# Performance work log

Measured on AMD Instinct MI355X. Metric: run time of the kernel, lower is better.

Reference implementation:

```python
import jax, jax.numpy as jnp
import numpy as np

H = 512
IN_DIM = 300
NUM_CLASSES = 45
LN_EPS = 1e-5


def _ln(x, g, b):
    m = jnp.mean(x, axis=-1, keepdims=True)
    v = jnp.mean((x - m) ** 2, axis=-1, keepdims=True)
    return (x - m) / jnp.sqrt(v + LN_EPS) * g + b


def _rnn_dir(xemb, Wx, bx, Wh, bh, ln_g, ln_b):
    # xemb: [B, T, H]; Wx/Wh: [3, H, H]; bx/bh: [3, H]; ln_g/ln_b: [3, H]
    B = xemb.shape[0]
    h_init = (jnp.zeros((B, H), xemb.dtype),) * 3

    def step(carry, xt):
        h0, h1, h2 = carry
        h0 = jnp.tanh(_ln(xt @ Wx[0] + bx[0] + h0 @ Wh[0] + bh[0], ln_g[0], ln_b[0]))
        h1 = jnp.tanh(_ln(h0 @ Wx[1] + bx[1] + h1 @ Wh[1] + bh[1], ln_g[1], ln_b[1]))
        h2 = jnp.tanh(_ln(h1 @ Wx[2] + bx[2] + h2 @ Wh[2] + bh[2], ln_g[2], ln_b[2]))
        return (h0, h1, h2), h2

    _, ys = jax.lax.scan(step, h_init, jnp.swapaxes(xemb, 0, 1))  # ys: [T, B, H]
    return jnp.swapaxes(ys, 0, 1)  # [B, T, H]


def setup_inputs() -> dict:
    key = jax.random.key(0)
    ks = jax.random.split(key, 20)
    B, T = 128, 256
    s_in = 1.0 / np.sqrt(IN_DIM)
    s_h = 1.0 / np.sqrt(H)
    inp = {
        "x": jax.random.normal(ks[0], (B, T, IN_DIM), jnp.float32),
        "reverse_x": jax.random.normal(ks[1], (B, T, IN_DIM), jnp.float32),
        "pad_start_index": jax.random.randint(ks[2], (B,), 0, T),
        "max_length": T,
        "W_emb": jax.random.uniform(ks[3], (IN_DIM, H), jnp.float32, -s_in, s_in),
        "b_emb": jax.random.uniform(ks[4], (H,), jnp.float32, -s_in, s_in),
        "Wx_l2r": jax.random.uniform(ks[5], (3, H, H), jnp.float32, -s_h, s_h),
        "bx_l2r": jax.random.uniform(ks[6], (3, H), jnp.float32, -s_h, s_h),
        "Wh_l2r": jax.random.uniform(ks[7], (3, H, H), jnp.float32, -s_h, s_h),
        "bh_l2r": jax.random.uniform(ks[8], (3, H), jnp.float32, -s_h, s_h),
        "Wx_r2l": jax.random.uniform(ks[9], (3, H, H), jnp.float32, -s_h, s_h),
        "bx_r2l": jax.random.uniform(ks[10], (3, H), jnp.float32, -s_h, s_h),
        "Wh_r2l": jax.random.uniform(ks[11], (3, H, H), jnp.float32, -s_h, s_h),
        "bh_r2l": jax.random.uniform(ks[12], (3, H), jnp.float32, -s_h, s_h),
        "ln_g": jnp.ones((3, H), jnp.float32),
        "ln_b": jnp.zeros((3, H), jnp.float32),
        "W_fc": jax.random.uniform(ks[13], (2 * H, NUM_CLASSES), jnp.float32, -1.0 / np.sqrt(2 * H), 1.0 / np.sqrt(2 * H)),
        "b_fc": jax.random.uniform(ks[14], (NUM_CLASSES,), jnp.float32, -1.0 / np.sqrt(2 * H), 1.0 / np.sqrt(2 * H)),
    }
    return inp


def reference(x, reverse_x, pad_start_index, max_length, W_emb, b_emb,
              Wx_l2r, bx_l2r, Wh_l2r, bh_l2r, Wx_r2l, bx_r2l, Wh_r2l, bh_r2l,
              ln_g, ln_b, W_fc, b_fc):
    x = x[:, :max_length]
    reverse_x = reverse_x[:, :max_length]
    x_l2r = x @ W_emb + b_emb           # [B, T, H]
    x_r2l = reverse_x @ W_emb + b_emb
    out_l2r = _rnn_dir(x_l2r, Wx_l2r, bx_l2r, Wh_l2r, bh_l2r, ln_g, ln_b)
    out_r2l = _rnn_dir(x_r2l, Wx_r2l, bx_r2l, Wh_r2l, bh_r2l, ln_g, ln_b)
    T = out_l2r.shape[1]
    j = jnp.arange(T)[None, :]
    p = pad_start_index[:, None]
    idx = jnp.where(j < p, p - j - 1, j)  # [B, T] gather index into r2l time axis
    r2l_g = jnp.take_along_axis(out_r2l, idx[:, :, None], axis=1)
    concat = jnp.concatenate([out_l2r, r2l_g], axis=-1)  # [B, T, 2H]
    logit = concat @ W_fc + b_fc
    return logit.reshape(-1, logit.shape[-1])
```

## Files before the change

kernel.cpp:

```cpp
#include <hip/hip_runtime.h>

#define Bdim 128
#define Tdim 256
#define Hdim 512
#define INdim 300
#define KXdim 320
#define NC 45
#define NTHR 256

typedef _Float16 h16;
typedef __attribute__((ext_vector_type(8))) _Float16 half8;
typedef __attribute__((ext_vector_type(4))) float float4v;
typedef unsigned long long u64;

__device__ __forceinline__ float fast_tanh(float v) {
    float e = __expf(2.0f * v);
    return 1.0f - 2.0f / (e + 1.0f);
}

__device__ __forceinline__ int ld_flag(const int* p) {
    return __hip_atomic_load((int*)p, __ATOMIC_RELAXED, __HIP_MEMORY_SCOPE_AGENT);
}
__device__ __forceinline__ void st_flag(int* p, int v) {
    __hip_atomic_store(p, v, __ATOMIC_RELAXED, __HIP_MEMORY_SCOPE_AGENT);
}
__device__ __forceinline__ float ld_f32c(const float* p) {
    return __hip_atomic_load((float*)p, __ATOMIC_RELAXED, __HIP_MEMORY_SCOPE_AGENT);
}
__device__ __forceinline__ void st_f32c(float* p, float v) {
    __hip_atomic_store(p, v, __ATOMIC_RELAXED, __HIP_MEMORY_SCOPE_AGENT);
}
__device__ __forceinline__ half8 ld16c(const h16* p) {
    union { u64 u[2]; half8 h; } r;
    const u64* q = (const u64*)p;
    r.u[0] = __hip_atomic_load((u64*)(q + 0), __ATOMIC_RELAXED, __HIP_MEMORY_SCOPE_AGENT);
    r.u[1] = __hip_atomic_load((u64*)(q + 1), __ATOMIC_RELAXED, __HIP_MEMORY_SCOPE_AGENT);
    return r.h;
}
__device__ __forceinline__ void st8c(h16* p, const uint* u) {
    uint* q = (uint*)p;
    __hip_atomic_store(q + 0, u[0], __ATOMIC_RELAXED, __HIP_MEMORY_SCOPE_AGENT);
    __hip_atomic_store(q + 1, u[1], __ATOMIC_RELAXED, __HIP_MEMORY_SCOPE_AGENT);
    __hip_atomic_store(q + 2, u[2], __ATOMIC_RELAXED, __HIP_MEMORY_SCOPE_AGENT);
    __hip_atomic_store(q + 3, u[3], __ATOMIC_RELAXED, __HIP_MEMORY_SCOPE_AGENT);
}

__global__ __launch_bounds__(NTHR) void prep1_kernel(
    const float* Wemb, const float* bemb,
    const float* Wx_l2r, const float* bx_l2r, const float* bh_l2r,
    const float* Wx_r2l, const float* bx_r2l, const float* bh_r2l,
    float* W0, float* cb)
{
    int gid = blockIdx.x * NTHR + threadIdx.x;
    const int nW0 = 2 * KXdim * Hdim;
    if (gid < nW0) {
        int dir = gid / (KXdim * Hdim);
        int rem = gid % (KXdim * Hdim);
        int i = rem / Hdim, h = rem % Hdim;
        const float* Wx = dir ? Wx_r2l : Wx_l2r;
        float s = 0.f;
        if (i < INdim) {
            for (int k = 0; k < Hdim; ++k)
                s += Wemb[i * Hdim + k] * Wx[k * Hdim + h];
        }
        W0[gid] = s;
    } else {
        int idx = gid - nW0;
        if (idx < 2 * 3 * Hdim) {
            int dir = idx / (3 * Hdim);
            int l = (idx / Hdim) % 3;
            int h = idx % Hdim;
            const float* Wx = dir ? Wx_r2l : Wx_l2r;
            const float* bx = dir ? bx_r2l : bx_l2r;
            const float* bh = dir ? bh_r2l : bh_l2r;
            float s = bx[l * Hdim + h] + bh[l * Hdim + h];
            if (l == 0) {
                for (int k = 0; k < Hdim; ++k)
                    s += bemb[k] * Wx[k * Hdim + h];
            }
            cb[idx] = s;
        }
    }
}

__global__ __launch_bounds__(NTHR) void pack_W_kernel(
    const float* W0,
    const float* Wx_l2r, const float* Wh_l2r,
    const float* Wx_r2l, const float* Wh_r2l,
    h16* Wfrag)
{
    int e = blockIdx.x * NTHR + threadIdx.x;
    if (e >= 6 * 16 * 32 * 2 * 64 * 8) return;
    int j    = e & 7;
    int lane = (e >> 3) & 63;
    int nt   = (e >> 9) & 1;
    int ks   = (e >> 10) & 31;
    int cs   = (e >> 15) & 15;
// ... 19 lines not shown
__global__ __launch_bounds__(NTHR) void pack_W0f_kernel(const float* W0, h16* W0f)
{
    int e = blockIdx.x * NTHR + threadIdx.x;
    if (e >= 2 * 32 * 10 * 64 * 8) return;
    int j    = e & 7;
    int lane = (e >> 3) & 63;
    int rest = e >> 9;
    int ks   = rest % 10;
    rest /= 10;
    int nt   = rest & 31;
    int dir  = rest >> 5;
    int k = ks * 32 + ((lane >> 4) * 8) + j;
    int n = nt * 16 + (lane & 15);
    W0f[e] = (h16)W0[(dir * KXdim + k) * Hdim + n];
}

__global__ __launch_bounds__(NTHR) void zx0_kernel(
    const float* __restrict__ x0, const float* __restrict__ x1,
    const h16* __restrict__ W0f, const float* __restrict__ cb,
    h16* __restrict__ zx0f)
{
    int bx = blockIdx.x;
    int t = bx & 255, mh = (bx >> 8) & 1, dir = bx >> 9;
    const int tid = threadIdx.x;
    __shared__ h16 xl[64 * 328];
    const float* xs = dir ? x1 : x0;
    for (int i = tid; i < 64 * 328; i += NTHR) {
        int r = i / 328, k = i - r * 328;
        int b = mh * 64 + r;
        float v = (k < INdim) ? xs[(b * Tdim + t) * INdim + k] : 0.f;
        xl[i] = (h16)v;
    }
    __syncthreads();
    int wave = tid >> 6, lane = tid & 63;
    int r15 = lane & 15, q = lane >> 4;
    for (int nt = 0; nt < 32; ++nt) {
        float4v acc = {0.f, 0.f, 0.f, 0.f};
        #pragma unroll
        for (int ks = 0; ks < 10; ++ks) {
            half8 af = *(const half8*)&xl[(wave * 16 + r15) * 328 + ks * 32 + q * 8];
            half8 bf = *(const half8*)&W0f[(((dir * 32 + nt) * 10 + ks) * 64 + lane) * 8];
            acc = __builtin_amdgcn_mfma_f32_16x16x32_f16(af, bf, acc, 0, 0, 0);
        }
        int col = nt * 16 + r15;
        float cbv = cb[(dir * 3 + 0) * Hdim + col];
        union { h16 h[4]; uint2 u2; } o;
        #pragma unroll
        for (int r = 0; r < 4; ++r) o.h[r] = (h16)(acc[r] + cbv);
        h16* dst = zx0f + (((( (size_t)dir * Tdim + t) * 32 + nt) * 8 + (mh * 4 + wave)) * 64 + lane) * 4;
        *(uint2*)dst = o.u2;
    }
}

__global__ __launch_bounds__(NTHR) void zeroinit_kernel(uint4* hfrag4, int* zdone, int* hdone)
{
    int gid = blockIdx.x * NTHR + threadIdx.x;
    if (gid < 6 * 8192) {
        int u = gid >> 13, i = gid & 8191;
        hfrag4[(size_t)(u * 4 + 3) * 8192 + i] = make_uint4(0, 0, 0, 0);
    }
    if (gid < 6 * 32) { zdone[gid] = 0; hdone[gid] = 0; }
}

struct PipeArgs {
    const h16* Wfrag;
    const h16* zx0f;
    const float* cb;
    const float* lng;
    const float* lnb;
    h16* hfrag;
    h16* h2;
    float* psum;
    float* psq;
    int* zdone;
    int* hdone;
};

__global__ __launch_bounds__(NTHR, 1) void rnn_pipe(PipeArgs a)
{
    const int blk = blockIdx.x, tid = threadIdx.x;
    const int u = blk & 7;
    if (u >= 6) return;
    const int widx = blk >> 3;
    const int mtblk = widx & 1, cs = widx >> 1;
    const int dir = u / 3, l = u % 3;
    const int wave = tid >> 6, lane = tid & 63;
    const int gmt = mtblk * 4 + wave;
    const int r15 = lane & 15, quad = lane >> 4;

    h16* __restrict__ hbuf = a.hfrag;
    float* __restrict__ psum = a.psum;
    float* __restrict__ psq  = a.psq;

    __shared__ h16 wlds[16384];
    __shared__ float lds_ps[64 * 16];
    __shared__ float lds_pq[64 * 16];
    __shared__ h16 lds_z[64 * 32];

    {
        const h16* src = a.Wfrag + (size_t)(u * 16 + cs) * 32768 + 16384;
        for (int i = tid * 8; i < 16384; i += NTHR * 8)
            *(uint4*)&wlds[i] = *(const uint4*)&src[i];
    }
    __syncthreads();

    const h16* wxg = a.Wfrag + (size_t)(u * 16 + cs) * 32768;
    const int colbase = cs * 32 + r15;
    const float cb0v = (l > 0) ? a.cb[(dir * 3 + l) * Hdim + colbase] : 0.f;
    const float cb1v = (l > 0) ? a.cb[(dir * 3 + l) * Hdim + colbase + 16] : 0.f;
    const float g0  = a.lng[l * Hdim + colbase];
    const float g1  = a.lng[l * Hdim + colbase + 16];
    const float bb0 = a.lnb[l * Hdim + colbase];
    const float bb1 = a.lnb[l * Hdim + colbase + 16];

    for (int t = 0; t < Tdim; ++t) {
        for (;;) {
            int ok = 1;
            if (tid < 32) {
                ok = (ld_flag(&a.hdone[u * 32 + tid]) >= t);
            } else if (tid >= 64 && tid < 96) {
                if (l > 0) ok = (ld_flag(&a.hdone[(u - 1) * 32 + (tid - 64)]) >= t + 1);
            } else if (tid >= 128 && tid < 160) {
                if (l < 2 && t >= 4) ok = (ld_flag(&a.zdone[(u + 1) * 32 + (tid - 128)]) >= t - 3);
            }
            if (__syncthreads_and(ok)) break;
            __builtin_amdgcn_s_sleep(2);
        }

        float4v acc0, acc1;
        const h16* basePrev = hbuf + (size_t)(u * 4 + ((t + 3) & 3)) * 65536;
        if (l == 0) {
            half8 afP[16];
            #pragma unroll
            for (int k = 0; k < 16; ++k)
                afP[k] = ld16c(&basePrev[((k * 8 + gmt) * 64 + lane) * 8]);
            const h16* zp = a.zx0f +
                (((((size_t)dir * Tdim + t) * 32 + cs * 2) * 8 + gmt) * 64 + lane) * 4;
            acc0[0] = (float)zp[0]; acc0[1] = (float)zp[1];
            acc0[2] = (float)zp[2]; acc0[3] = (float)zp[3];
            const h16* zp1 = zp + 2048;
            acc1[0] = (float)zp1[0]; acc1[1] = (float)zp1[1];
            acc1[2] = (float)zp1[2]; acc1[3] = (float)zp1[3];
            #pragma unroll
            for (int ks = 0; ks < 16; ++ks) {
                half8 bh0 = *(const half8*)&wlds[((ks * 2 + 0) * 64 + lane) * 8];
                half8 bh1 = *(const half8*)&wlds[((ks * 2 + 1) * 64 + lane) * 8];
                acc0 = __builtin_amdgcn_mfma_f32_16x16x32_f16(afP[ks], bh0, acc0, 0, 0, 0);
                acc1 = __builtin_amdgcn_mfma_f32_16x16x32_f16(afP[ks], bh1, acc1, 0, 0, 0);
            }
        } else {
            const h16* baseLow = hbuf + (size_t)((u - 1) * 4 + (t & 3)) * 65536;
            half8 afL[16], afP[16];
            #pragma unroll
            for (int k = 0; k < 16; ++k)
                afL[k] = ld16c(&baseLow[((k * 8 + gmt) * 64 + lane) * 8]);
            #pragma unroll
            for (int k = 0; k < 16; ++k)
                afP[k] = ld16c(&basePrev[((k * 8 + gmt) * 64 + lane) * 8]);
            acc0 = (float4v){0.f, 0.f, 0.f, 0.f};
            acc1 = (float4v){0.f, 0.f, 0.f, 0.f};
            #pragma unroll
            for (int ks = 0; ks < 16; ++ks) {
                half8 bx0 = *(const half8*)&wxg[((ks * 2 + 0) * 64 + lane) * 8];
                half8 bx1 = *(const half8*)&wxg[((ks * 2 + 1) * 64 + lane) * 8];
                half8 bh0 = *(const half8*)&wlds[((ks * 2 + 0) * 64 + lane) * 8];
                half8 bh1 = *(const half8*)&wlds[((ks * 2 + 1) * 64 + lane) * 8];
                acc0 = __builtin_amdgcn_mfma_f32_16x16x32_f16(afL[ks], bx0, acc0, 0, 0, 0);
                acc1 = __builtin_amdgcn_mfma_f32_16x16x32_f16(afL[ks], bx1, acc1, 0, 0, 0);
                acc0 = __builtin_amdgcn_mfma_f32_16x16x32_f16(afP[ks], bh0, acc0, 0, 0, 0);
                acc1 = __builtin_amdgcn_mfma_f32_16x16x32_f16(afP[ks], bh1, acc1, 0, 0, 0);
            }
        }

        float z0[4], z1[4];
        #pragma unroll
        for (int r = 0; r < 4; ++r) {
            z0[r] = acc0[r] + cb0v;
            z1[r] = acc1[r] + cb1v;
            float s = z0[r] + z1[r];
            float q2 = z0[r] * z0[r] + z1[r] * z1[r];
            s += __shfl_xor(s, 1);  q2 += __shfl_xor(q2, 1);
            s += __shfl_xor(s, 2);  q2 += __shfl_xor(q2, 2);
            s += __shfl_xor(s, 4);  q2 += __shfl_xor(q2, 4);
            s += __shfl_xor(s, 8);  q2 += __shfl_xor(q2, 8);
            if (r15 == 0) {
                int b = mtblk * 64 + wave * 16 + quad * 4 + r;
                st_f32c(&psum[(u * Bdim + b) * 16 + cs], s);
                st_f32c(&psq [(u * Bdim + b) * 16 + cs], q2);
            }
        }
        __syncthreads();
        if (tid == 0) st_flag(&a.zdone[u * 32 + widx], t + 1);

        for (;;) {
            int ok = 1;
            if (tid < 32) ok = (ld_flag(&a.zdone[u * 32 + tid]) >= t + 1);
            if (__syncthreads_and(ok)) break;
            __builtin_amdgcn_s_sleep(2);
        }

        {
            int flat = tid * 4;
            int rl = flat >> 4, c = flat & 15;
            int b = mtblk * 64 + rl;
            #pragma unroll
            for (int j = 0; j < 4; ++j) {
                lds_ps[rl * 16 + c + j] = ld_f32c(&psum[(u * Bdim + b) * 16 + c + j]);
                lds_pq[rl * 16 + c + j] = ld_f32c(&psq [(u * Bdim + b) * 16 + c + j]);
            }
        }
        __syncthreads();
        #pragma unroll
        for (int r = 0; r < 4; ++r) {
            int lrow = wave * 16 + quad * 4 + r;
            float sm = 0.f, sq = 0.f;
            #pragma unroll
            for (int c = 0; c < 16; ++c) { sm += lds_ps[lrow * 16 + c]; sq += lds_pq[lrow * 16 + c]; }
            float m = sm * (1.0f / Hdim);
            float var = sq * (1.0f / Hdim) - m * m;
            float rstd = rsqrtf(var + 1e-5f);
            lds_z[lrow * 32 + r15]      = (h16)fast_tanh((z0[r] - m) * rstd * g0 + bb0);
            lds_z[lrow * 32 + r15 + 16] = (h16)fast_tanh((z1[r] - m) * rstd * g1 + bb1);
        }
        __syncthreads();

        {
            int b_l = tid >> 2, c0 = (tid & 3) * 8;
            union { h16 h[8]; uint u4[4]; uint4 v; } o;
            const h16* src = &lds_z[b_l * 32 + c0];
            #pragma unroll
            for (int j = 0; j < 8; ++j) o.h[j] = src[j];
            int mt = mtblk * 4 + (b_l >> 4);
            int lane2 = (b_l & 15) | ((tid & 3) << 4);
            h16* dst = hbuf + (size_t)(u * 4 + (t & 3)) * 65536 +
                       ((size_t)((cs * 8 + mt) * 64 + lane2)) * 8;
            st8c(dst, o.u4);
            if (l == 2) {
                h16* d2 = a.h2 + (((size_t)dir * Tdim + t) * Bdim + mtblk * 64 + b_l) * Hdim
                          + cs * 32 + c0;
                *(uint4*)d2 = o.v;
            }
        }
        __syncthreads();
        if (tid == 0) st_flag(&a.hdone[u * 32 + widx], t + 1);
    }
}

__global__ __launch_bounds__(NTHR) void fc_kernel(
    const h16* __restrict__ h2, const int* __restrict__ pad,
    const float* __restrict__ Wfc, const float* __restrict__ bfc,
    float* __restrict__ out)
{
    __shared__ float sA[64 * 68];
    __shared__ float sB[64 * 48];
    const int blk = blockIdx.x, tid = threadIdx.x;
    const int b = blk >> 2;
    const int j0 = (blk & 3) * 64;
    const int p = pad[b];
    const int rg = tid >> 4;
    const int c0 = (tid & 15) * 3;
    float acc[4][3] = {};

    for (int k0 = 0; k0 < 2 * Hdim; k0 += 64) {
        {
            int rr = tid >> 2;
            int kp = (tid & 3) * 16;
            int j = j0 + rr;
            const h16* src;
            if (k0 < Hdim) {
                src = h2 + (((size_t)0 * Tdim + j) * Bdim + b) * Hdim + k0 + kp;
            } else {
                int idx = (j < p) ? (p - j - 1) : j;
                src = h2 + (((size_t)1 * Tdim + idx) * Bdim + b) * Hdim + (k0 - Hdim) + kp;
            }
            union { uint4 u4; h16 h[8]; } w0, w1;
            w0.u4 = *(const uint4*)src;
            w1.u4 = *(const uint4*)(src + 8);
            #pragma unroll
            for (int i = 0; i < 8; ++i) {
                sA[rr * 68 + kp + i]     = (float)w0.h[i];
                sA[rr * 68 + kp + 8 + i] = (float)w1.h[i];
            }
        }
        for (int e = tid; e < 64 * 48; e += NTHR) {
            int kk = e / 48, c = e - kk * 48;
            sB[e] = (c < NC) ? Wfc[(k0 + kk) * NC + c] : 0.f;
        }
        __syncthreads();
        for (int kk = 0; kk < 64; ++kk) {
            float b0 = sB[kk * 48 + c0 + 0];
            float b1 = sB[kk * 48 + c0 + 1];
            float b2 = sB[kk * 48 + c0 + 2];
            #pragma unroll
            for (int i = 0; i < 4; ++i) {
                float av = sA[(rg * 4 + i) * 68 + kk];
                acc[i][0] += av * b0; acc[i][1] += av * b1; acc[i][2] += av * b2;
            }
        }
        __syncthreads();
    }
    #pragma unroll
    for (int i = 0; i < 4; ++i) {
        int r = blk * 64 + rg * 4 + i;
        #pragma unroll
        for (int jj = 0; jj < 3; ++jj) {
            int c = c0 + jj;
            if (c < NC) out[r * NC + c] = acc[i][jj] + bfc[c];
        }
    }
}

extern "C" void kernel_launch(void* const* d_in, const int* in_sizes, int n_in,
                              void* d_out, int out_size, void* d_ws, size_t ws_size,
                              hipStream_t stream) {
    const float* x      = (const float*)d_in[0];
    const float* rx     = (const float*)d_in[1];
    const int*   pad    = (const int*)d_in[2];
    const float* Wemb   = (const float*)d_in[4];
    const float* bemb   = (const float*)d_in[5];
    const float* Wx_l2r = (const float*)d_in[6];
    const float* bx_l2r = (const float*)d_in[7];
    const float* Wh_l2r = (const float*)d_in[8];
    const float* bh_l2r = (const float*)d_in[9];
    const float* Wx_r2l = (const float*)d_in[10];
    const float* bx_r2l = (const float*)d_in[11];
    const float* Wh_r2l = (const float*)d_in[12];
    const float* bh_r2l = (const float*)d_in[13];
    const float* lng    = (const float*)d_in[14];
    const float* lnb    = (const float*)d_in[15];
    const float* Wfc    = (const float*)d_in[16];
    const float* bfc    = (const float*)d_in[17];

    char* base = (char*)d_ws;
    size_t off = 0;
    auto alloc = [&](size_t bytes) { char* p = base + off; off += (bytes + 255) & ~(size_t)255; return p; };
    h16*   zx0f  = (h16*)  alloc((size_t)2 * Tdim * 32 * 8 * 64 * 4 * 2);
    h16*   h2    = (h16*)  alloc((size_t)2 * Tdim * Bdim * Hdim * 2);
    h16*   Wfrag = (h16*)  alloc((size_t)6 * 16 * 32768 * 2);
    h16*   W0f   = (h16*)  alloc((size_t)2 * 32 * 10 * 64 * 8 * 2);
    h16*   hfrag = (h16*)  alloc((size_t)6 * 4 * 65536 * 2);
    float* psum  = (float*)alloc((size_t)6 * Bdim * 16 * 4);
    float* psq   = (float*)alloc((size_t)6 * Bdim * 16 * 4);
    float* W0    = (float*)alloc((size_t)2 * KXdim * Hdim * 4);
    float* cb    = (float*)alloc((size_t)2 * 3 * Hdim * 4);
    int*   zdone = (int*)  alloc(192 * 4);
    int*   hdone = (int*)  alloc(192 * 4);

    prep1_kernel<<<(2 * KXdim * Hdim + 2 * 3 * Hdim) / NTHR, NTHR, 0, stream>>>(
        Wemb, bemb, Wx_l2r, bx_l2r, bh_l2r, Wx_r2l, bx_r2l, bh_r2l, W0, cb);

    pack_W_kernel<<<(6 * 16 * 32 * 2 * 64 * 8) / NTHR, NTHR, 0, stream>>>(
        W0, Wx_l2r, Wh_l2r, Wx_r2l, Wh_r2l, Wfrag);

    pack_W0f_kernel<<<(2 * 32 * 10 * 64 * 8) / NTHR, NTHR, 0, stream>>>(W0, W0f);

    zx0_kernel<<<1024, NTHR, 0, stream>>>(x, rx, W0f, cb, zx0f);

    zeroinit_kernel<<<(6 * 8192 + NTHR - 1) / NTHR, NTHR, 0, stream>>>(
        (uint4*)hfrag, zdone, hdone);

    PipeArgs a;
    a.Wfrag = Wfrag; a.zx0f = zx0f; a.cb = cb; a.lng = lng; a.lnb = lnb;
    a.hfrag = hfrag; a.h2 = h2; a.psum = psum; a.psq = psq;
    a.zdone = zdone; a.hdone = hdone;
    void* kargs[] = { &a };
    hipLaunchCooperativeKernel((void*)rnn_pipe, dim3(256), dim3(NTHR), kargs, 0, stream);

    fc_kernel<<<(Bdim * Tdim) / 64, NTHR, 0, stream>>>(h2, pad, Wfc, bfc, (float*)d_out);
}
```

Before: 3.805 ms.

## Defer LayerNorm+tanh to consumers to remove second per-step grid barrier

Producers now publish raw pre-activation z and per-row partial sums and sums of squares into a 4-deep ring, and signal once per step. Consumers compute the mean and rstd themselves and apply LayerNorm plus tanh on the fly while building MFMA operands. This removes the second cross-block wait per timestep, which was needed to gather LN statistics before writing h, and it also pads the flags to avoid false sharing. In exchange, every consumer block recomputes the normalization and tanh for all of K, adding VALU work. The last layer's h2 output now lags one step and needs an epilogue.

```diff
diff --git a/kernel.cpp b/kernel.cpp
--- a/kernel.cpp
+++ b/kernel.cpp
@@ -7,6 +7,7 @@
 #define KXdim 320
 #define NC 45
 #define NTHR 256
+#define FPAD 16
 
 typedef _Float16 h16;
 typedef __attribute__((ext_vector_type(8))) _Float16 half8;
@@ -23,9 +24,6 @@
 }
 __device__ __forceinline__ void st_flag(int* p, int v) {
     __hip_atomic_store(p, v, __ATOMIC_RELAXED, __HIP_MEMORY_SCOPE_AGENT);
-}
-__device__ __forceinline__ float ld_f32c(const float* p) {
-    return __hip_atomic_load((float*)p, __ATOMIC_RELAXED, __HIP_MEMORY_SCOPE_AGENT);
 }
 __device__ __forceinline__ void st_f32c(float* p, float v) {
     __hip_atomic_store(p, v, __ATOMIC_RELAXED, __HIP_MEMORY_SCOPE_AGENT);
@@ -168,14 +166,10 @@
     }
 }
 
-__global__ __launch_bounds__(NTHR) void zeroinit_kernel(uint4* hfrag4, int* zdone, int* hdone)
+__global__ __launch_bounds__(NTHR) void zeroinit_kernel(int* zdone)
 {
     int gid = blockIdx.x * NTHR + threadIdx.x;
-    if (gid < 6 * 8192) {
-        int u = gid >> 13, i = gid & 8191;
-        hfrag4[(size_t)(u * 4 + 3) * 8192 + i] = make_uint4(0, 0, 0, 0);
-    }
-    if (gid < 6 * 32) { zdone[gid] = 0; hdone[gid] = 0; }
+    if (gid < 6 * 32 * FPAD) zdone[gid] = 0;
 }
 
 struct PipeArgs {
@@ -184,13 +178,49 @@
     const float* cb;
     const float* lng;
     const float* lnb;
-    h16* hfrag;
+    h16* zbuf;
     h16* h2;
-    float* psum;
-    float* psq;
+    float* pstat;
     int* zdone;
-    int* hdone;
 };
+
+__device__ __forceinline__ void compute_mr(float* dst, const float* ps, int mtblk, int tid)
+{
+    if (tid < 64) {
+        const u64* q = (const u64*)(ps + (mtblk * 64 + tid) * 32);
+        float s = 0.f, qq = 0.f;
+        #pragma unroll
+        for (int i = 0; i < 8; ++i) {
+            union { u64 w; float f[2]; } v;
+            v.w = __hip_atomic_load((u64*)(q + i), __ATOMIC_RELAXED, __HIP_MEMORY_SCOPE_AGENT);
+            s += v.f[0] + v.f[1];
+        }
+        #pragma unroll
+        for (int i = 8; i < 16; ++i) {
+            union { u64 w; float f[2]; } v;
+            v.w = __hip_atomic_load((u64*)(q + i), __ATOMIC_RELAXED, __HIP_MEMORY_SCOPE_AGENT);
+            qq += v.f[0] + v.f[1];
+        }
+        float m = s * (1.0f / Hdim);
+        float var = qq * (1.0f / Hdim) - m * m;
+        float rstd = rsqrtf(var + 1e-5f);
+        dst[tid * 2 + 0] = rstd;
+        dst[tid * 2 + 1] = -m * rstd;
+    }
+}
+
+__device__ __forceinline__ half8 cvt_h(half8 zf, float A, float C,
+                                       const float* g, const float* bb)
+{
+    union { h16 h[8]; half8 v; } o;
+    #pragma unroll
+    for (int j = 0; j < 8; ++j) {
+        float z = (float)zf[j];
+        float x = __builtin_fmaf(__builtin_fmaf(z, A, C), g[j], bb[j]);
+        o.h[j] = (h16)fast_tanh(x);
+    }
+    return o.v;
+}
 
 __global__ __launch_bounds__(NTHR, 1) void rnn_pipe(PipeArgs a)
 {
@@ -204,13 +234,11 @@
     const int gmt = mtblk * 4 + wave;
     const int r15 = lane & 15, quad = lane >> 4;
 
-    h16* __restrict__ hbuf = a.hfrag;
-    float* __restrict__ psum = a.psum;
-    float* __restrict__ psq  = a.psq;
-
     __shared__ h16 wlds[16384];
-    __shared__ float lds_ps[64 * 16];
-    __shared__ float lds_pq[64 * 16];
+    __shared__ float lnpP[2 * Hdim];
+    __shared__ float lnpL[2 * Hdim];
+    __shared__ float mrP[128];
+    __shared__ float mrL[128];
     __shared__ h16 lds_z[64 * 32];
 
     {
@@ -218,73 +246,93 @@
         for (int i = tid * 8; i < 16384; i += NTHR * 8)
             *(uint4*)&wlds[i] = *(const uint4*)&src[i];
     }
+    for (int i = tid; i < Hdim; i += NTHR) {
+        lnpP[i]        = a.lng[l * Hdim + i];
+        lnpP[Hdim + i] = a.lnb[l * Hdim + i];
+        if (l > 0) {
+            lnpL[i]        = a.lng[(l - 1) * Hdim + i];
+            lnpL[Hdim + i] = a.lnb[(l - 1) * Hdim + i];
+        }
+    }
     __syncthreads();
 
     const h16* wxg = a.Wfrag + (size_t)(u * 16 + cs) * 32768;
     const int colbase = cs * 32 + r15;
     const float cb0v = (l > 0) ? a.cb[(dir * 3 + l) * Hdim + colbase] : 0.f;
     const float cb1v = (l > 0) ? a.cb[(dir * 3 + l) * Hdim + colbase + 16] : 0.f;
-    const float g0  = a.lng[l * Hdim + colbase];
-    const float g1  = a.lng[l * Hdim + colbase + 16];
-    const float bb0 = a.lnb[l * Hdim + colbase];
-    const float bb1 = a.lnb[l * Hdim + colbase + 16];
 
     for (int t = 0; t < Tdim; ++t) {
         for (;;) {
             int ok = 1;
             if (tid < 32) {
-                ok = (ld_flag(&a.hdone[u * 32 + tid]) >= t);
+                if (l > 0) ok = (ld_flag(&a.zdone[((u - 1) * 32 + tid) * FPAD]) >= t + 1);
             } else if (tid >= 64 && tid < 96) {
-                if (l > 0) ok = (ld_flag(&a.hdone[(u - 1) * 32 + (tid - 64)]) >= t + 1);
-            } else if (tid >= 128 && tid < 160) {
-                if (l < 2 && t >= 4) ok = (ld_flag(&a.zdone[(u + 1) * 32 + (tid - 128)]) >= t - 3);
+                if (l < 2 && t >= 4) ok = (ld_flag(&a.zdone[((u + 1) * 32 + (tid - 64)) * FPAD]) >= t - 3);
             }
             if (__syncthreads_and(ok)) break;
             __builtin_amdgcn_s_sleep(2);
         }
 
         float4v acc0, acc1;
-        const h16* basePrev = hbuf + (size_t)(u * 4 + ((t + 3) & 3)) * 65536;
         if (l == 0) {
-            half8 afP[16];
-            #pragma unroll
-            for (int k = 0; k < 16; ++k)
-                afP[k] = ld16c(&basePrev[((k * 8 + gmt) * 64 + lane) * 8]);
             const h16* zp = a.zx0f +
                 (((((size_t)dir * Tdim + t) * 32 + cs * 2) * 8 + gmt) * 64 + lane) * 4;
-            acc0[0] = (float)zp[0]; acc0[1] = (float)zp[1];
-            acc0[2] = (float)zp[2]; acc0[3] = (float)zp[3];
-            const h16* zp1 = zp + 2048;
-            acc1[0] = (float)zp1[0]; acc1[1] = (float)zp1[1];
-            acc1[2] = (float)zp1[2]; acc1[3] = (float)zp1[3];
+            union { uint2 w; h16 h[4]; } v0, v1;
+            v0.w = *(const uint2*)zp;
+            v1.w = *(const uint2*)(zp + 2048);
+            #pragma unroll
+            for (int r = 0; r < 4; ++r) { acc0[r] = (float)v0.h[r]; acc1[r] = (float)v1.h[r]; }
+        } else {
+            const h16* zL = a.zbuf + (size_t)((u - 1) * 4 + (t & 3)) * 65536;
+            half8 af[16];
+            #pragma unroll
+            for (int ks = 0; ks < 16; ++ks)
+                af[ks] = ld16c(&zL[((ks * 8 + gmt) * 64 + lane) * 8]);
+            compute_mr(mrL, a.pstat + (size_t)((u - 1) * 4 + (t & 3)) * 4096, mtblk, tid);
+            __syncthreads();
+            const float A = mrL[(wave * 16 + r15) * 2 + 0];
+            const float C = mrL[(wave * 16 + r15) * 2 + 1];
+            acc0 = (float4v){0.f, 0.f, 0.f, 0.f};
+            acc1 = (float4v){0.f, 0.f, 0.f, 0.f};
             #pragma unroll
             for (int ks = 0; ks < 16; ++ks) {
+                int k0 = ks * 32 + quad * 8;
+                half8 hf = cvt_h(af[ks], A, C, &lnpL[k0], &lnpL[Hdim + k0]);
+                half8 bx0 = *(const half8*)&wxg[((ks * 2 + 0) * 64 + lane) * 8];
+                half8 bx1 = *(const half8*)&wxg[((ks * 2 + 1) * 64 + lane) * 8];
+                acc0 = __builtin_amdgcn_mfma_f32_16x16x32_f16(hf, bx0, acc0, 0, 0, 0);
+                acc1 = __builtin_amdgcn_mfma_f32_16x16x32_f16(hf, bx1, acc1, 0, 0, 0);
+            }
+        }
+
+        for (;;) {
+            int ok = 1;
+            if (tid < 32) ok = (ld_flag(&a.zdone[(u * 32 + tid) * FPAD]) >= t);
+            if (__syncthreads_and(ok)) break;
+            __builtin_amdgcn_s_sleep(2);
+        }
+        if (t > 0) {
+            const h16* zP = a.zbuf + (size_t)(u * 4 + ((t + 3) & 3)) * 65536;
+            half8 af[16];
+            #pragma unroll
+            for (int ks = 0; ks < 16; ++ks)
+                af[ks] = ld16c(&zP[((ks * 8 + gmt) * 64 + lane) * 8]);
+            compute_mr(mrP, a.pstat + (size_t)(u * 4 + ((t + 3) & 3)) * 4096, mtblk, tid);
+            __syncthreads();
+            const float A = mrP[(wave * 16 + r15) * 2 + 0];
+            const float C = mrP[(wave * 16 + r15) * 2 + 1];
+            #pragma unroll
+            for (int ks = 0; ks < 16; ++ks) {
+                int k0 = ks * 32 + quad * 8;
+                half8 hf = cvt_h(af[ks], A, C, &lnpP[k0], &lnpP[Hdim + k0]);
+                if (l == 2 && ks == cs) {
+                    union { half8 v; uint4 q; } w; w.v = hf;
+                    *(uint4*)&a.h2[(((size_t)dir * Tdim + (t - 1)) * Bdim + gmt * 16 + r15) * Hdim + k0] = w.q;
+                }
                 half8 bh0 = *(const half8*)&wlds[((ks * 2 + 0) * 64 + lane) * 8];
                 half8 bh1 = *(const half8*)&wlds[((ks * 2 + 1) * 64 + lane) * 8];
-                acc0 = __builtin_amdgcn_mfma_f32_16x16x32_f16(afP[ks], bh0, acc0, 0, 0, 0);
-                acc1 = __builtin_amdgcn_mfma_f32_16x16x32_f16(afP[ks], bh1, acc1, 0, 0, 0);
-            }
-        } else {
-            const h16* baseLow = hbuf + (size_t)((u - 1) * 4 + (t & 3)) * 65536;
-            half8 afL[16], afP[16];
-            #pragma unroll
-            for (int k = 0; k < 16; ++k)
-                afL[k] = ld16c(&baseLow[((k * 8 + gmt) * 64 + lane) * 8]);
-            #pragma unroll
-            for (int k = 0; k < 16; ++k)
-                afP[k] = ld16c(&basePrev[((k * 8 + gmt) * 64 + lane) * 8]);
-            acc0 = (float4v){0.f, 0.f, 0.f, 0.f};
-            acc1 = (float4v){0.f, 0.f, 0.f, 0.f};
-            #pragma unroll
-            for (int ks = 0; ks < 16; ++ks) {
-                half8 bx0 = *(const half8*)&wxg[((ks * 2 + 0) * 64 + lane) * 8];
-                half8 bx1 = *(const half8*)&wxg[((ks * 2 + 1) * 64 + lane) * 8];
-                half8 bh0 = *(const half8*)&wlds[((ks * 2 + 0) * 64 + lane) * 8];
-                half8 bh1 = *(const half8*)&wlds[((ks * 2 + 1) * 64 + lane) * 8];
-                acc0 = __builtin_amdgcn_mfma_f32_16x16x32_f16(afL[ks], bx0, acc0, 0, 0, 0);
-                acc1 = __builtin_amdgcn_mfma_f32_16x16x32_f16(afL[ks], bx1, acc1, 0, 0, 0);
-                acc0 = __builtin_amdgcn_mfma_f32_16x16x32_f16(afP[ks], bh0, acc0, 0, 0, 0);
-                acc1 = __builtin_amdgcn_mfma_f32_16x16x32_f16(afP[ks], bh1, acc1, 0, 0, 0);
+                acc0 = __builtin_amdgcn_mfma_f32_16x16x32_f16(hf, bh0, acc0, 0, 0, 0);
+                acc1 = __builtin_amdgcn_mfma_f32_16x16x32_f16(hf, bh1, acc1, 0, 0, 0);
             }
         }
 
@@ -301,64 +349,52 @@
             s += __shfl_xor(s, 8);  q2 += __shfl_xor(q2, 8);
             if (r15 == 0) {
                 int b = mtblk * 64 + wave * 16 + quad * 4 + r;
-                st_f32c(&psum[(u * Bdim + b) * 16 + cs], s);
-                st_f32c(&psq [(u * Bdim + b) * 16 + cs], q2);
-            }
+                float* pr = a.pstat + (size_t)(u * 4 + (t & 3)) * 4096 + b * 32;
+                st_f32c(pr + cs, s);
+                st_f32c(pr + 16 + cs, q2);
+            }
+        }
+        #pragma unroll
+        for (int r = 0; r < 4; ++r) {
+            int lrow = wave * 16 + quad * 4 + r;
+            lds_z[lrow * 32 + r15]      = (h16)z0[r];
+            lds_z[lrow * 32 + 16 + r15] = (h16)z1[r];
         }
         __syncthreads();
-        if (tid == 0) st_flag(&a.zdone[u * 32 + widx], t + 1);
-
+        {
+            int b_l = tid >> 2, c0 = (tid & 3) * 8;
+            union { h16 h[8]; uint u4[4]; } o;
+            const h16* srcz = &lds_z[b_l * 32 + c0];
+            #pragma unroll
+            for (int j = 0; j < 8; ++j) o.h[j] = srcz[j];
+            int mt = mtblk * 4 + (b_l >> 4);
+            int lane2 = (b_l & 15) | ((tid & 3) << 4);
+            h16* dst = a.zbuf + (size_t)(u * 4 + (t & 3)) * 65536 +
+                       ((size_t)((cs * 8 + mt) * 64 + lane2)) * 8;
+            st8c(dst, o.u4);
+        }
+        __syncthreads();
+        if (tid == 0) st_flag(&a.zdone[(u * 32 + widx) * FPAD], t + 1);
+    }
+
+    if (l == 2) {
         for (;;) {
             int ok = 1;
-            if (tid < 32) ok = (ld_flag(&a.zdone[u * 32 + tid]) >= t + 1);
+            if (tid < 32) ok = (ld_flag(&a.zdone[(u * 32 + tid) * FPAD]) >= Tdim);
             if (__syncthreads_and(ok)) break;
             __builtin_amdgcn_s_sleep(2);
         }
-
-        {
-            int flat = tid * 4;
-            int rl = flat >> 4, c = flat & 15;
-            int b = mtblk * 64 + rl;
-            #pragma unroll
-            for (int j = 0; j < 4; ++j) {
-                lds_ps[rl * 16 + c + j] = ld_f32c(&psum[(u * Bdim + b) * 16 + c + j]);
-                lds_pq[rl * 16 + c + j] = ld_f32c(&psq [(u * Bdim + b) * 16 + c + j]);
-            }
-        }
+        compute_mr(mrP, a.pstat + (size_t)(u * 4 + 3) * 4096, mtblk, tid);
         __syncthreads();
-        #pragma unroll
-        for (int r = 0; r < 4; ++r) {
-            int lrow = wave * 16 + quad * 4 + r;
-            float sm = 0.f, sq = 0.f;
-            #pragma unroll
-            for (int c = 0; c < 16; ++c) { sm += lds_ps[lrow * 16 + c]; sq += lds_pq[lrow * 16 + c]; }
-            float m = sm * (1.0f / Hdim);
-            float var = sq * (1.0f / Hdim) - m * m;
-            float rstd = rsqrtf(var + 1e-5f);
-            lds_z[lrow * 32 + r15]      = (h16)fast_tanh((z0[r] - m) * rstd * g0 + bb0);
-            lds_z[lrow * 32 + r15 + 16] = (h16)fast_tanh((z1[r] - m) * rstd * g1 + bb1);
-        }
-        __syncthreads();
-
-        {
-            int b_l = tid >> 2, c0 = (tid & 3) * 8;
-            union { h16 h[8]; uint u4[4]; uint4 v; } o;
-            const h16* src = &lds_z[b_l * 32 + c0];
-            #pragma unroll
-            for (int j = 0; j < 8; ++j) o.h[j] = src[j];
-            int mt = mtblk * 4 + (b_l >> 4);
-            int lane2 = (b_l & 15) | ((tid & 3) << 4);
-            h16* dst = hbuf + (size_t)(u * 4 + (t & 3)) * 65536 +
-                       ((size_t)((cs * 8 + mt) * 64 + lane2)) * 8;
-            st8c(dst, o.u4);
-            if (l == 2) {
-                h16* d2 = a.h2 + (((size_t)dir * Tdim + t) * Bdim + mtblk * 64 + b_l) * Hdim
-                          + cs * 32 + c0;
-                *(uint4*)d2 = o.v;
-            }
-        }
-        __syncthreads();
-        if (tid == 0) st_flag(&a.hdone[u * 32 + widx], t + 1);
+        const h16* zP = a.zbuf + (size_t)(u * 4 + 3) * 65536;
+        const float A = mrP[(wave * 16 + r15) * 2 + 0];
+        const float C = mrP[(wave * 16 + r15) * 2 + 1];
+        int ks = cs;
+        int k0 = ks * 32 + quad * 8;
+        half8 zf = ld16c(&zP[((ks * 8 + gmt) * 64 + lane) * 8]);
+        half8 hf = cvt_h(zf, A, C, &lnpP[k0], &lnpP[Hdim + k0]);
+        union { half8 v; uint4 q; } w; w.v = hf;
+        *(uint4*)&a.h2[(((size_t)dir * Tdim + (Tdim - 1)) * Bdim + gmt * 16 + r15) * Hdim + k0] = w.q;
     }
 }
 
@@ -454,13 +490,11 @@
     h16*   h2    = (h16*)  alloc((size_t)2 * Tdim * Bdim * Hdim * 2);
     h16*   Wfrag = (h16*)  alloc((size_t)6 * 16 * 32768 * 2);
     h16*   W0f   = (h16*)  alloc((size_t)2 * 32 * 10 * 64 * 8 * 2);
-    h16*   hfrag = (h16*)  alloc((size_t)6 * 4 * 65536 * 2);
-    float* psum  = (float*)alloc((size_t)6 * Bdim * 16 * 4);
-    float* psq   = (float*)alloc((size_t)6 * Bdim * 16 * 4);
+    h16*   zbuf  = (h16*)  alloc((size_t)6 * 4 * 65536 * 2);
+    float* pstat = (float*)alloc((size_t)6 * 4 * Bdim * 32 * 4);
     float* W0    = (float*)alloc((size_t)2 * KXdim * Hdim * 4);
     float* cb    = (float*)alloc((size_t)2 * 3 * Hdim * 4);
-    int*   zdone = (int*)  alloc(192 * 4);
-    int*   hdone = (int*)  alloc(192 * 4);
+    int*   zdone = (int*)  alloc((size_t)6 * 32 * FPAD * 4);
 
     prep1_kernel<<<(2 * KXdim * Hdim + 2 * 3 * Hdim) / NTHR, NTHR, 0, stream>>>(
         Wemb, bemb, Wx_l2r, bx_l2r, bh_l2r, Wx_r2l, bx_r2l, bh_r2l, W0, cb);
@@ -472,13 +506,11 @@
 
     zx0_kernel<<<1024, NTHR, 0, stream>>>(x, rx, W0f, cb, zx0f);
 
-    zeroinit_kernel<<<(6 * 8192 + NTHR - 1) / NTHR, NTHR, 0, stream>>>(
-        (uint4*)hfrag, zdone, hdone);
+    zeroinit_kernel<<<(6 * 32 * FPAD + NTHR - 1) / NTHR, NTHR, 0, stream>>>(zdone);
 
     PipeArgs a;
     a.Wfrag = Wfrag; a.zx0f = zx0f; a.cb = cb; a.lng = lng; a.lnb = lnb;
-    a.hfrag = hfrag; a.h2 = h2; a.psum = psum; a.psq = psq;
-    a.zdone = zdone; a.hdone = hdone;
+    a.zbuf = zbuf; a.h2 = h2; a.pstat = pstat; a.zdone = zdone;
     void* kargs[] = { &a };
     hipLaunchCooperativeKernel((void*)rnn_pipe, dim3(256), dim3(NTHR), kargs, 0, stream);
 
```

Result: slower. 4.969 ms (+30.6%).

## Restructure RNN pipeline: full weights in LDS, padded flags, per-half-batch sync groups

Applied to the files above, without the earlier changes.

The recurrent pipeline kernel now loads both Wx and Wh slices into LDS instead of streaming Wx from global memory. The grid shrinks from 256 to 192 blocks with no idle blocks. Hidden-state fragments and layernorm partial stats use a new layout, and stats are stored as packed 64-bit pairs. Sync flags are padded to separate cache lines, use release stores, and are grouped per batch half so each block waits on 16 peers instead of 32. The t=0 hidden matmul is skipped instead of reading a zeroed buffer. Layer-0 backpressure now reuses hdone rather than a separate zdone, and the larger LDS footprint could limit overlap.

```diff
diff --git a/kernel.cpp b/kernel.cpp
--- a/kernel.cpp
+++ b/kernel.cpp
@@ -7,28 +7,18 @@
 #define KXdim 320
 #define NC 45
 #define NTHR 256
+#define FPAD 16
 
 typedef _Float16 h16;
 typedef __attribute__((ext_vector_type(8))) _Float16 half8;
 typedef __attribute__((ext_vector_type(4))) float float4v;
 typedef unsigned long long u64;
 
-__device__ __forceinline__ float fast_tanh(float v) {
-    float e = __expf(2.0f * v);
-    return 1.0f - 2.0f / (e + 1.0f);
-}
-
 __device__ __forceinline__ int ld_flag(const int* p) {
     return __hip_atomic_load((int*)p, __ATOMIC_RELAXED, __HIP_MEMORY_SCOPE_AGENT);
 }
-__device__ __forceinline__ void st_flag(int* p, int v) {
-    __hip_atomic_store(p, v, __ATOMIC_RELAXED, __HIP_MEMORY_SCOPE_AGENT);
-}
-__device__ __forceinline__ float ld_f32c(const float* p) {
-    return __hip_atomic_load((float*)p, __ATOMIC_RELAXED, __HIP_MEMORY_SCOPE_AGENT);
-}
-__device__ __forceinline__ void st_f32c(float* p, float v) {
-    __hip_atomic_store(p, v, __ATOMIC_RELAXED, __HIP_MEMORY_SCOPE_AGENT);
+__device__ __forceinline__ void st_flag_rel(int* p, int v) {
+    __hip_atomic_store(p, v, __ATOMIC_RELEASE, __HIP_MEMORY_SCOPE_AGENT);
 }
 __device__ __forceinline__ half8 ld16c(const h16* p) {
     union { u64 u[2]; half8 h; } r;
@@ -43,6 +33,15 @@
     __hip_atomic_store(q + 1, u[1], __ATOMIC_RELAXED, __HIP_MEMORY_SCOPE_AGENT);
     __hip_atomic_store(q + 2, u[2], __ATOMIC_RELAXED, __HIP_MEMORY_SCOPE_AGENT);
     __hip_atomic_store(q + 3, u[3], __ATOMIC_RELAXED, __HIP_MEMORY_SCOPE_AGENT);
+}
+__device__ __forceinline__ void st_ps(float* p, float s, float q) {
+    union { float f[2]; u64 u; } v; v.f[0] = s; v.f[1] = q;
+    __hip_atomic_store((u64*)p, v.u, __ATOMIC_RELAXED, __HIP_MEMORY_SCOPE_AGENT);
+}
+__device__ __forceinline__ void ld_ps(const float* p, float& s, float& q) {
+    union { float f[2]; u64 u; } v;
+    v.u = __hip_atomic_load((u64*)p, __ATOMIC_RELAXED, __HIP_MEMORY_SCOPE_AGENT);
+    s = v.f[0]; q = v.f[1];
 }
 
 __global__ __launch_bounds__(NTHR) void prep1_kernel(
@@ -168,14 +167,10 @@
     }
 }
 
-__global__ __launch_bounds__(NTHR) void zeroinit_kernel(uint4* hfrag4, int* zdone, int* hdone)
+__global__ __launch_bounds__(NTHR) void zeroinit_kernel(int* hdone, int* sdone)
 {
     int gid = blockIdx.x * NTHR + threadIdx.x;
-    if (gid < 6 * 8192) {
-        int u = gid >> 13, i = gid & 8191;
-        hfrag4[(size_t)(u * 4 + 3) * 8192 + i] = make_uint4(0, 0, 0, 0);
-    }
-    if (gid < 6 * 32) { zdone[gid] = 0; hdone[gid] = 0; }
+    if (gid < 192 * FPAD) { hdone[gid] = 0; sdone[gid] = 0; }
 }
 
 struct PipeArgs {
@@ -184,181 +179,181 @@
     const float* cb;
     const float* lng;
     const float* lnb;
-    h16* hfrag;
+    h16* hbuf;
+    float* pstat;
     h16* h2;
-    float* psum;
-    float* psq;
-    int* zdone;
     int* hdone;
+    int* sdone;
 };
 
-__global__ __launch_bounds__(NTHR, 1) void rnn_pipe(PipeArgs a)
+__device__ __forceinline__ size_t hb_idx(int u, int slot, int rh, int kf, int mt) {
+    return ((((size_t)(u * 4 + slot) * 2 + rh) * 16 + kf) * 4 + mt) * 512;
+}
+
+__global__ __launch_bounds__(NTHR, 2) void rnn_pipe(PipeArgs a)
 {
     const int blk = blockIdx.x, tid = threadIdx.x;
-    const int u = blk & 7;
-    if (u >= 6) return;
-    const int widx = blk >> 3;
-    const int mtblk = widx & 1, cs = widx >> 1;
+    const int w = tid >> 6, lane = tid & 63;
+    const int r15 = lane & 15, quad = lane >> 4;
+    const int u = blk >> 5, rh = (blk >> 4) & 1, cs = blk & 15;
     const int dir = u / 3, l = u % 3;
-    const int wave = tid >> 6, lane = tid & 63;
-    const int gmt = mtblk * 4 + wave;
-    const int r15 = lane & 15, quad = lane >> 4;
-
-    h16* __restrict__ hbuf = a.hfrag;
-    float* __restrict__ psum = a.psum;
-    float* __restrict__ psq  = a.psq;
-
-    __shared__ h16 wlds[16384];
-    __shared__ float lds_ps[64 * 16];
-    __shared__ float lds_pq[64 * 16];
-    __shared__ h16 lds_z[64 * 32];
+
+    __shared__ h16 wlds[32768];
+    __shared__ h16 tile[4][512];
+    __shared__ float mr[64][2];
 
     {
-        const h16* src = a.Wfrag + (size_t)(u * 16 + cs) * 32768 + 16384;
-        for (int i = tid * 8; i < 16384; i += NTHR * 8)
-            *(uint4*)&wlds[i] = *(const uint4*)&src[i];
+        const h16* wsrc = a.Wfrag + (size_t)(u * 16 + cs) * 32768;
+        for (int i = tid * 8; i < 32768; i += NTHR * 8)
+            *(uint4*)&wlds[i] = *(const uint4*)&wsrc[i];
+    }
+    float g2[2], b2[2], cbv[2];
+    #pragma unroll
+    for (int n = 0; n < 2; ++n) {
+        int col = cs * 32 + n * 16 + r15;
+        g2[n] = 2.0f * a.lng[l * Hdim + col];
+        b2[n] = 2.0f * a.lnb[l * Hdim + col];
+        cbv[n] = (l > 0) ? a.cb[(dir * 3 + l) * Hdim + col] : 0.f;
     }
     __syncthreads();
 
-    const h16* wxg = a.Wfrag + (size_t)(u * 16 + cs) * 32768;
-    const int colbase = cs * 32 + r15;
-    const float cb0v = (l > 0) ? a.cb[(dir * 3 + l) * Hdim + colbase] : 0.f;
-    const float cb1v = (l > 0) ? a.cb[(dir * 3 + l) * Hdim + colbase + 16] : 0.f;
-    const float g0  = a.lng[l * Hdim + colbase];
-    const float g1  = a.lng[l * Hdim + colbase + 16];
-    const float bb0 = a.lnb[l * Hdim + colbase];
-    const float bb1 = a.lnb[l * Hdim + colbase + 16];
+    const int fl = ((u * 2 + rh) * 16 + cs) * FPAD;
+    const int gmt = rh * 4 + w;
 
     for (int t = 0; t < Tdim; ++t) {
         for (;;) {
             int ok = 1;
-            if (tid < 32) {
-                ok = (ld_flag(&a.hdone[u * 32 + tid]) >= t);
-            } else if (tid >= 64 && tid < 96) {
-                if (l > 0) ok = (ld_flag(&a.hdone[(u - 1) * 32 + (tid - 64)]) >= t + 1);
-            } else if (tid >= 128 && tid < 160) {
-                if (l < 2 && t >= 4) ok = (ld_flag(&a.zdone[(u + 1) * 32 + (tid - 128)]) >= t - 3);
+            if (tid < 16) {
+                if (t > 0) ok = (ld_flag(&a.hdone[((u * 2 + rh) * 16 + tid) * FPAD]) >= t);
+            } else if (tid >= 64 && tid < 80) {
+                if (l > 0) ok = (ld_flag(&a.hdone[(((u - 1) * 2 + rh) * 16 + (tid - 64)) * FPAD]) >= t + 1);
+            } else if (tid >= 128 && tid < 144) {
+                if (l < 2 && t >= 4) ok = (ld_flag(&a.hdone[(((u + 1) * 2 + rh) * 16 + (tid - 128)) * FPAD]) >= t - 3);
             }
             if (__syncthreads_and(ok)) break;
-            __builtin_amdgcn_s_sleep(2);
-        }
+            __builtin_amdgcn_s_sleep(1);
+        }
+        asm volatile("" ::: "memory");
 
         float4v acc0, acc1;
-        const h16* basePrev = hbuf + (size_t)(u * 4 + ((t + 3) & 3)) * 65536;
         if (l == 0) {
-            half8 afP[16];
-            #pragma unroll
-            for (int k = 0; k < 16; ++k)
-                afP[k] = ld16c(&basePrev[((k * 8 + gmt) * 64 + lane) * 8]);
             const h16* zp = a.zx0f +
-                (((((size_t)dir * Tdim + t) * 32 + cs * 2) * 8 + gmt) * 64 + lane) * 4;
-            acc0[0] = (float)zp[0]; acc0[1] = (float)zp[1];
-            acc0[2] = (float)zp[2]; acc0[3] = (float)zp[3];
-            const h16* zp1 = zp + 2048;
-            acc1[0] = (float)zp1[0]; acc1[1] = (float)zp1[1];
-            acc1[2] = (float)zp1[2]; acc1[3] = (float)zp1[3];
-            #pragma unroll
-            for (int ks = 0; ks < 16; ++ks) {
-                half8 bh0 = *(const half8*)&wlds[((ks * 2 + 0) * 64 + lane) * 8];
-                half8 bh1 = *(const half8*)&wlds[((ks * 2 + 1) * 64 + lane) * 8];
-                acc0 = __builtin_amdgcn_mfma_f32_16x16x32_f16(afP[ks], bh0, acc0, 0, 0, 0);
-                acc1 = __builtin_amdgcn_mfma_f32_16x16x32_f16(afP[ks], bh1, acc1, 0, 0, 0);
-            }
+                ((((size_t)dir * Tdim + t) * 32 + cs * 2) * 8 + gmt) * 256 + lane * 4;
+            union { uint2 uu; h16 hh[4]; } v0, v1;
+            v0.uu = *(const uint2*)zp;
+            v1.uu = *(const uint2*)(zp + 2048);
+            #pragma unroll
+            for (int r = 0; r < 4; ++r) { acc0[r] = (float)v0.hh[r]; acc1[r] = (float)v1.hh[r]; }
         } else {
-            const h16* baseLow = hbuf + (size_t)((u - 1) * 4 + (t & 3)) * 65536;
-            half8 afL[16], afP[16];
-            #pragma unroll
-            for (int k = 0; k < 16; ++k)
-                afL[k] = ld16c(&baseLow[((k * 8 + gmt) * 64 + lane) * 8]);
-            #pragma unroll
-            for (int k = 0; k < 16; ++k)
-                afP[k] = ld16c(&basePrev[((k * 8 + gmt) * 64 + lane) * 8]);
             acc0 = (float4v){0.f, 0.f, 0.f, 0.f};
             acc1 = (float4v){0.f, 0.f, 0.f, 0.f};
+        }
+
+        half8 afL[16], afP[16];
+        if (l > 0) {
+            const h16* hbL = a.hbuf + hb_idx(u - 1, t & 3, rh, 0, w) + lane * 8;
+            #pragma unroll
+            for (int ks = 0; ks < 16; ++ks)
+                afL[ks] = ld16c(hbL + (size_t)ks * 2048);
+        }
+        if (t > 0) {
+            const h16* hbP = a.hbuf + hb_idx(u, (t + 3) & 3, rh, 0, w) + lane * 8;
+            #pragma unroll
+            for (int ks = 0; ks < 16; ++ks)
+                afP[ks] = ld16c(hbP + (size_t)ks * 2048);
+        }
+        if (l > 0) {
             #pragma unroll
             for (int ks = 0; ks < 16; ++ks) {
-                half8 bx0 = *(const half8*)&wxg[((ks * 2 + 0) * 64 + lane) * 8];
-                half8 bx1 = *(const half8*)&wxg[((ks * 2 + 1) * 64 + lane) * 8];
-                half8 bh0 = *(const half8*)&wlds[((ks * 2 + 0) * 64 + lane) * 8];
-                half8 bh1 = *(const half8*)&wlds[((ks * 2 + 1) * 64 + lane) * 8];
-                acc0 = __builtin_amdgcn_mfma_f32_16x16x32_f16(afL[ks], bx0, acc0, 0, 0, 0);
-                acc1 = __builtin_amdgcn_mfma_f32_16x16x32_f16(afL[ks], bx1, acc1, 0, 0, 0);
-                acc0 = __builtin_amdgcn_mfma_f32_16x16x32_f16(afP[ks], bh0, acc0, 0, 0, 0);
-                acc1 = __builtin_amdgcn_mfma_f32_16x16x32_f16(afP[ks], bh1, acc1, 0, 0, 0);
-            }
-        }
-
-        float z0[4], z1[4];
+                half8 b0 = *(const half8*)&wlds[((ks * 2 + 0) * 64 + lane) * 8];
+                half8 b1 = *(const half8*)&wlds[((ks * 2 + 1) * 64 + lane) * 8];
+                acc0 = __builtin_amdgcn_mfma_f32_16x16x32_f16(afL[ks], b0, acc0, 0, 0, 0);
+                acc1 = __builtin_amdgcn_mfma_f32_16x16x32_f16(afL[ks], b1, acc1, 0, 0, 0);
+            }
+        }
+        if (t > 0) {
+            #pragma unroll
+            for (int ks = 0; ks < 16; ++ks) {
+                half8 b0 = *(const half8*)&wlds[(((ks + 16) * 2 + 0) * 64 + lane) * 8];
+                half8 b1 = *(const half8*)&wlds[(((ks + 16) * 2 + 1) * 64 + lane) * 8];
+                acc0 = __builtin_amdgcn_mfma_f32_16x16x32_f16(afP[ks], b0, acc0, 0, 0, 0);
+                acc1 = __builtin_amdgcn_mfma_f32_16x16x32_f16(afP[ks], b1, acc1, 0, 0, 0);
+            }
+        }
+        #pragma unroll
+        for (int r = 0; r < 4; ++r) { acc0[r] += cbv[0]; acc1[r] += cbv[1]; }
+
+        {
+            float* pb = a.pstat + ((((size_t)(u * 4 + (t & 3)) * 2 + rh) * 16 + cs) * 64) * 2;
+            #pragma unroll
+            for (int r = 0; r < 4; ++r) {
+                float s = acc0[r] + acc1[r];
+                float q = __builtin_fmaf(acc0[r], acc0[r], acc1[r] * acc1[r]);
+                s += __shfl_xor(s, 1); q += __shfl_xor(q, 1);
+                s += __shfl_xor(s, 2); q += __shfl_xor(q, 2);
+                s += __shfl_xor(s, 4); q += __shfl_xor(q, 4);
+                s += __shfl_xor(s, 8); q += __shfl_xor(q, 8);
+                if (r15 == 0) {
+                    int row = w * 16 + quad * 4 + r;
+                    st_ps(pb + row * 2, s, q);
+                }
+            }
+        }
+        __syncthreads();
+        if (tid == 0) st_flag_rel(&a.sdone[fl], t + 1);
+
+        for (;;) {
+            int ok = 1;
+            if (tid < 16) ok = (ld_flag(&a.sdone[((u * 2 + rh) * 16 + tid) * FPAD]) >= t + 1);
+            if (__syncthreads_and(ok)) break;
+            __builtin_amdgcn_s_sleep(1);
+        }
+        asm volatile("" ::: "memory");
+
+        if (tid < 64) {
+            const float* pb = a.pstat + (((size_t)(u * 4 + (t & 3)) * 2 + rh) * 16) * 128;
+            float ss = 0.f, qq = 0.f;
+            #pragma unroll
+            for (int c = 0; c < 16; ++c) {
+                float s, q;
+                ld_ps(pb + (c * 64 + tid) * 2, s, q);
+                ss += s; qq += q;
+            }
+            float m = ss * (1.0f / Hdim);
+            float var = qq * (1.0f / Hdim) - m * m;
+            float rstd = rsqrtf(var + 1e-5f);
+            mr[tid][0] = rstd;
+            mr[tid][1] = -m * rstd;
+        }
+        __syncthreads();
+
         #pragma unroll
         for (int r = 0; r < 4; ++r) {
-            z0[r] = acc0[r] + cb0v;
-            z1[r] = acc1[r] + cb1v;
-            float s = z0[r] + z1[r];
-            float q2 = z0[r] * z0[r] + z1[r] * z1[r];
-            s += __shfl_xor(s, 1);  q2 += __shfl_xor(q2, 1);
-            s += __shfl_xor(s, 2);  q2 += __shfl_xor(q2, 2);
-            s += __shfl_xor(s, 4);  q2 += __shfl_xor(q2, 4);
-            s += __shfl_xor(s, 8);  q2 += __shfl_xor(q2, 8);
-            if (r15 == 0) {
-                int b = mtblk * 64 + wave * 16 + quad * 4 + r;
-                st_f32c(&psum[(u * Bdim + b) * 16 + cs], s);
-                st_f32c(&psq [(u * Bdim + b) * 16 + cs], q2);
-            }
+            int row = quad * 4 + r;
+            int grow = w * 16 + row;
+            float A = mr[grow][0], C = mr[grow][1];
+            float x0 = __builtin_fmaf(__builtin_fmaf(acc0[r], A, C), g2[0], b2[0]);
+            float x1 = __builtin_fmaf(__builtin_fmaf(acc1[r], A, C), g2[1], b2[1]);
+            float E0 = __expf(x0), E1 = __expf(x1);
+            int sw = (row >> 2) << 3;
+            tile[w][row * 32 + ((r15) ^ sw)]      = (h16)(1.0f - __fdividef(2.0f, E0 + 1.0f));
+            tile[w][row * 32 + ((16 + r15) ^ sw)] = (h16)(1.0f - __fdividef(2.0f, E1 + 1.0f));
+        }
+        {
+            int row = lane & 15;
+            int cb2 = (quad * 8) ^ ((row >> 2) << 3);
+            union { half8 v; uint uu[4]; } o;
+            o.v = *(const half8*)&tile[w][row * 32 + cb2];
+            st8c(a.hbuf + hb_idx(u, t & 3, rh, cs, w) + lane * 8, o.uu);
+        }
+        if (l == 2) {
+            int row = lane >> 2, cg = (lane & 3) * 8;
+            uint4 v = *(const uint4*)&tile[w][row * 32 + (cg ^ ((row >> 2) << 3))];
+            int grow = rh * 64 + w * 16 + row;
+            *(uint4*)&a.h2[(((size_t)dir * Tdim + t) * Bdim + grow) * Hdim + cs * 32 + cg] = v;
         }
         __syncthreads();
-        if (tid == 0) st_flag(&a.zdone[u * 32 + widx], t + 1);
-
-        for (;;) {
-            int ok = 1;
-            if (tid < 32) ok = (ld_flag(&a.zdone[u * 32 + tid]) >= t + 1);
-            if (__syncthreads_and(ok)) break;
-            __builtin_amdgcn_s_sleep(2);
-        }
-
-        {
-            int flat = tid * 4;
-            int rl = flat >> 4, c = flat & 15;
-            int b = mtblk * 64 + rl;
-            #pragma unroll
-            for (int j = 0; j < 4; ++j) {
-                lds_ps[rl * 16 + c + j] = ld_f32c(&psum[(u * Bdim + b) * 16 + c + j]);
-                lds_pq[rl * 16 + c + j] = ld_f32c(&psq [(u * Bdim + b) * 16 + c + j]);
-            }
-        }
-        __syncthreads();
-        #pragma unroll
-        for (int r = 0; r < 4; ++r) {
-            int lrow = wave * 16 + quad * 4 + r;
-            float sm = 0.f, sq = 0.f;
-            #pragma unroll
-            for (int c = 0; c < 16; ++c) { sm += lds_ps[lrow * 16 + c]; sq += lds_pq[lrow * 16 + c]; }
-            float m = sm * (1.0f / Hdim);
-            float var = sq * (1.0f / Hdim) - m * m;
-            float rstd = rsqrtf(var + 1e-5f);
-            lds_z[lrow * 32 + r15]      = (h16)fast_tanh((z0[r] - m) * rstd * g0 + bb0);
-            lds_z[lrow * 32 + r15 + 16] = (h16)fast_tanh((z1[r] - m) * rstd * g1 + bb1);
-        }
-        __syncthreads();
-
-        {
-            int b_l = tid >> 2, c0 = (tid & 3) * 8;
-            union { h16 h[8]; uint u4[4]; uint4 v; } o;
-            const h16* src = &lds_z[b_l * 32 + c0];
-            #pragma unroll
-            for (int j = 0; j < 8; ++j) o.h[j] = src[j];
-            int mt = mtblk * 4 + (b_l >> 4);
-            int lane2 = (b_l & 15) | ((tid & 3) << 4);
-            h16* dst = hbuf + (size_t)(u * 4 + (t & 3)) * 65536 +
-                       ((size_t)((cs * 8 + mt) * 64 + lane2)) * 8;
-            st8c(dst, o.u4);
-            if (l == 2) {
-                h16* d2 = a.h2 + (((size_t)dir * Tdim + t) * Bdim + mtblk * 64 + b_l) * Hdim
-                          + cs * 32 + c0;
-                *(uint4*)d2 = o.v;
-            }
-        }
-        __syncthreads();
-        if (tid == 0) st_flag(&a.hdone[u * 32 + widx], t + 1);
+        if (tid == 0) st_flag_rel(&a.hdone[fl], t + 1);
     }
 }
 
@@ -454,13 +449,12 @@
     h16*   h2    = (h16*)  alloc((size_t)2 * Tdim * Bdim * Hdim * 2);
     h16*   Wfrag = (h16*)  alloc((size_t)6 * 16 * 32768 * 2);
     h16*   W0f   = (h16*)  alloc((size_t)2 * 32 * 10 * 64 * 8 * 2);
-    h16*   hfrag = (h16*)  alloc((size_t)6 * 4 * 65536 * 2);
-    float* psum  = (float*)alloc((size_t)6 * Bdim * 16 * 4);
-    float* psq   = (float*)alloc((size_t)6 * Bdim * 16 * 4);
+    h16*   hbuf  = (h16*)  alloc((size_t)6 * 4 * 2 * 16 * 4 * 512 * 2);
+    float* pstat = (float*)alloc((size_t)6 * 4 * 2 * 16 * 64 * 2 * 4);
     float* W0    = (float*)alloc((size_t)2 * KXdim * Hdim * 4);
     float* cb    = (float*)alloc((size_t)2 * 3 * Hdim * 4);
-    int*   zdone = (int*)  alloc(192 * 4);
-    int*   hdone = (int*)  alloc(192 * 4);
+    int*   hdone = (int*)  alloc((size_t)192 * FPAD * 4);
+    int*   sdone = (int*)  alloc((size_t)192 * FPAD * 4);
 
     prep1_kernel<<<(2 * KXdim * Hdim + 2 * 3 * Hdim) / NTHR, NTHR, 0, stream>>>(
         Wemb, bemb, Wx_l2r, bx_l2r, bh_l2r, Wx_r2l, bx_r2l, bh_r2l, W0, cb);
@@ -472,15 +466,14 @@
 
     zx0_kernel<<<1024, NTHR, 0, stream>>>(x, rx, W0f, cb, zx0f);
 
-    zeroinit_kernel<<<(6 * 8192 + NTHR - 1) / NTHR, NTHR, 0, stream>>>(
-        (uint4*)hfrag, zdone, hdone);
+    zeroinit_kernel<<<(192 * FPAD + NTHR - 1) / NTHR, NTHR, 0, stream>>>(hdone, sdone);
 
     PipeArgs a;
     a.Wfrag = Wfrag; a.zx0f = zx0f; a.cb = cb; a.lng = lng; a.lnb = lnb;
-    a.hfrag = hfrag; a.h2 = h2; a.psum = psum; a.psq = psq;
-    a.zdone = zdone; a.hdone = hdone;
+    a.hbuf = hbuf; a.pstat = pstat; a.h2 = h2;
+    a.hdone = hdone; a.sdone = sdone;
     void* kargs[] = { &a };
-    hipLaunchCooperativeKernel((void*)rnn_pipe, dim3(256), dim3(NTHR), kargs, 0, stream);
+    hipLaunchCooperativeKernel((void*)rnn_pipe, dim3(192), dim3(NTHR), kargs, 0, stream);
 
     fc_kernel<<<(Bdim * Tdim) / 64, NTHR, 0, stream>>>(h2, pad, Wfc, bfc, (float*)d_out);
 }
```

After: 4.256 ms. 11.8% more time.
